# Kernel optimization log

Measured on AMD Instinct MI355X. Metric: run time of the kernel, lower is better.

## Reference

```python
import jax, jax.numpy as jnp
import numpy as np

N_EMBD = 512
HEAD_SIZE = 64
T = 4096
B = 4


def setup_inputs() -> dict:
    key = jax.random.key(0)
    kx, kq, kk, kv = jax.random.split(key, 4)
    x = jax.random.normal(kx, (B, T, N_EMBD), dtype=jnp.float32)
    # torch nn.Linear(n_embd, head_size, bias=False): weight [head_size, n_embd];
    # stored here transposed as [n_embd, head_size] so projection is x @ W.
    s = 1.0 / np.sqrt(N_EMBD)
    Wq = jax.random.uniform(kq, (N_EMBD, HEAD_SIZE), jnp.float32, -s, s)
    Wk = jax.random.uniform(kk, (N_EMBD, HEAD_SIZE), jnp.float32, -s, s)
    Wv = jax.random.uniform(kv, (N_EMBD, HEAD_SIZE), jnp.float32, -s, s)
    return {"x": x, "Wq": Wq, "Wk": Wk, "Wv": Wv}


def reference(x, Wq, Wk, Wv):
    Bq, Tq, C = x.shape
    q = x @ Wq  # [B,T,H]
    k = x @ Wk  # [B,T,H]
    v = x @ Wv  # [B,T,H]
    # NOTE: original scales by C**-0.5 with C = n_embd (input dim), not head_size.
    wei = jnp.einsum('bqh,bkh->bqk', q, k) * (C ** -0.5)  # [B,T,T]
    causal = jnp.tril(jnp.ones((Tq, Tq), dtype=bool))
    wei = jnp.where(causal, wei, -jnp.inf)
    wei = jax.nn.softmax(wei, axis=-1)
    # dropout p=0.0 -> identity (eval-mode deterministic baseline)
    out = jnp.einsum('bqk,bkh->bqh', wei, v)  # [B,T,H]
    return out
```

## Files before the change

kernel.cpp:

```cpp
#include <hip/hip_runtime.h>
#include <hip/hip_bf16.h>
#include <math.h>

#define T_SEQ 4096
#define NBATCH 4
#define C_EMB 512
#define HEAD 64
#define CHUNK 8
#define EPB 144

typedef __attribute__((ext_vector_type(8))) short short8;
typedef __attribute__((ext_vector_type(4))) short short4v;
typedef __attribute__((ext_vector_type(4))) float f32x4;

#define C2 (0.044194173824159216f * 1.44269504088896340736f)

__device__ __forceinline__ unsigned short f2bf(float f) {
    union { float f; unsigned u; } v; v.f = f;
    unsigned u = v.u;
    u += 0x7FFF + ((u >> 16) & 1);
    return (unsigned short)(u >> 16);
}
__device__ __forceinline__ unsigned pk2bf(float a, float b) {
    __hip_bfloat162 h = __float22bfloat162_rn(make_float2(a, b));
    return *(unsigned*)&h;
}
__device__ __forceinline__ float bf2f(unsigned short u) {
    union { unsigned u; float f; } v; v.u = ((unsigned)u) << 16;
    return v.f;
}

#define GLD_LDS16(gp, lp)                                                     \
    __builtin_amdgcn_global_load_lds(                                         \
        (const __attribute__((address_space(1))) void*)(gp),                  \
        (__attribute__((address_space(3))) void*)(lp), 16, 0, 0)

__global__ __launch_bounds__(64) void wcvt_kernel(
    const float* __restrict__ Wq, const float* __restrict__ Wk,
    const float* __restrict__ Wv, unsigned short* __restrict__ wt2)
{
    const int gid  = blockIdx.x * 64 + threadIdx.x;
    const int lane = gid & 63;
    int rest = gid >> 6;
    const int kc   = rest & 1; rest >>= 1;
    const int tile = rest % 12;
    const int c    = rest / 12;
    const float* W = (tile < 4) ? Wq : (tile < 8) ? Wk : Wv;
    const int n  = (tile & 3) * 16 + (lane & 15);
    const int k0 = c * 64 + kc * 32 + (lane >> 4) * 8;
    unsigned short tmp[8];
#pragma unroll
    for (int i = 0; i < 8; ++i) tmp[i] = f2bf(W[(size_t)(k0 + i) * HEAD + n]);
    *(short8*)(wt2 + (size_t)gid * 8) = *(short8*)tmp;
}

__global__ __launch_bounds__(512, 4) void proj_kernel(
    const float* __restrict__ x,
    const unsigned short* __restrict__ wt2,
    unsigned short* __restrict__ qout,
    unsigned short* __restrict__ kout,
    unsigned short* __restrict__ vt)
{
    __shared__ unsigned short Wl[2][12288];
    __shared__ unsigned short Xl[2][32][72];

    const int tid  = threadIdx.x;
    const int wave = tid >> 6;
    const int lane = tid & 63;
    const int l16  = lane & 15;
    const int quad = lane >> 4;
    const int row0 = blockIdx.x * 32;
    const int mq   = wave & 1;
    const int ng   = wave >> 1;

    const bool xst = tid < 256;
    const int xrow = tid >> 3;
    const int xc8  = (tid & 7) * 8;

    f32x4 acc[3];
#pragma unroll
    for (int j = 0; j < 3; ++j) acc[j] = (f32x4){0.f, 0.f, 0.f, 0.f};

#pragma unroll
    for (int m = 0; m < 3; ++m)
        GLD_LDS16(wt2 + (size_t)(m * 4096 + wave * 512 + lane * 8),
                  &Wl[0][m * 4096 + wave * 512]);
    if (xst) {
        const float* xs = x + (size_t)(row0 + xrow) * C_EMB + xc8;
        float4 a = *(const float4*)(xs);
        float4 b = *(const float4*)(xs + 4);
        int4 ai = make_int4((int)pk2bf(a.x, a.y), (int)pk2bf(a.z, a.w),
                            (int)pk2bf(b.x, b.y), (int)pk2bf(b.z, b.w));
        *(short8*)&Xl[0][xrow][xc8] = *(short8*)&ai;
    }
    __syncthreads();

    for (int c = 0; c < 8; ++c) {
        const int bb = c & 1;
        if (c < 7) {
            const int nb = bb ^ 1;
            const size_t g0 = (size_t)(c + 1) * 12288;
#pragma unroll
            for (int m = 0; m < 3; ++m)
                GLD_LDS16(wt2 + g0 + (size_t)(m * 4096 + wave * 512 + lane * 8),
                          &Wl[nb][m * 4096 + wave * 512]);
            if (xst) {
                const float* xs = x + (size_t)(row0 + xrow) * C_EMB + (c + 1) * 64 + xc8;
                float4 a = *(const float4*)(xs);
                float4 b = *(const float4*)(xs + 4);
                int4 ai = make_int4((int)pk2bf(a.x, a.y), (int)pk2bf(a.z, a.w),
                                    (int)pk2bf(b.x, b.y), (int)pk2bf(b.z, b.w));
                *(short8*)&Xl[nb][xrow][xc8] = *(short8*)&ai;
            }
        }

#pragma unroll
        for (int kc = 0; kc < 2; ++kc) {
            short8 a0 = *(const short8*)&Xl[bb][mq * 16 + l16][kc * 32 + quad * 8];
#pragma unroll
            for (int j = 0; j < 3; ++j) {
                const int ct = ng * 3 + j;
                short8 bfr = *(const short8*)&Wl[bb][(ct * 128 + kc * 64 + lane) * 8];
                acc[j] = __builtin_amdgcn_mfma_f32_16x16x32_bf16(a0, bfr, acc[j], 0, 0, 0);
            }
        }
        __syncthreads();
    }

    unsigned short (*Vsh)[40] = (unsigned short (*)[40]) & Xl[0][0][0];
#pragma unroll
    for (int j = 0; j < 3; ++j) {
        const int ct = ng * 3 + j;
        const int m  = ct >> 2;
        const int n  = ct & 3;
#pragma unroll
        for (int r = 0; r < 4; ++r) {
            const int row = row0 + mq * 16 + quad * 4 + r;
            if (m == 0)
                qout[(size_t)row * HEAD + n * 16 + l16] = f2bf(acc[j][r] * C2);
            else if (m == 1)
                kout[(size_t)row * HEAD + n * 16 + l16] = f2bf(acc[j][r]);
            else
                Vsh[n * 16 + l16][mq * 16 + quad * 4 + r] = f2bf(acc[j][r]);
        }
    }
    __syncthreads();
    if (tid < 256) {
        int h  = tid >> 2;
        int tc = (tid & 3) * 8;
        int b  = row0 >> 12;
        int t0 = row0 & (T_SEQ - 1);
        unsigned short* dst = vt + ((size_t)(b * HEAD + h)) * T_SEQ + t0 + tc;
        *(short8*)dst = *(const short8*)&Vsh[h][tc];
    }
}

__device__ __forceinline__ void stage_v8(unsigned short (*Vbuf)[72], int sr, int pos0,
                                         short8 v0) {
    *(short4v*)&Vbuf[sr][pos0]     = __builtin_shufflevector(v0, v0, 0, 1, 2, 3);
    *(short4v*)&Vbuf[sr][pos0 + 8] = __builtin_shufflevector(v0, v0, 4, 5, 6, 7);
}

__global__ __launch_bounds__(512, 4) void attn1_kernel(
    const unsigned short* __restrict__ qb,
    const unsigned short* __restrict__ kb,
    const unsigned short* __restrict__ vt,
    unsigned short* __restrict__ po,
    float* __restrict__ pl)
{
    __shared__ unsigned short Ks[2][64][72];
    __shared__ unsigned short Vs[2][64][72];

    const int tid  = threadIdx.x;
    const int wave = tid >> 6;
    const int lane = tid & 63;
    const int l16  = lane & 15;
    const int quad = lane >> 4;

    const int b = blockIdx.x / EPB;
    const int e = (EPB - 1) - (blockIdx.x % EPB);
    int g = 0;
#pragma unroll
    for (int gg = 1; gg < 8; ++gg) if (e >= 2 * gg * (gg + 1)) g = gg;
    const int rem = e - 2 * g * (g + 1);
    const int t   = rem / (g + 1);
    const int c   = rem - t * (g + 1);
    const int Q   = 4 * g + t;

    const size_t base = (size_t)b * T_SEQ;
    const int qrow0 = Q * 128 + wave * 16;
    const int qrow  = qrow0 + l16;
    short8 aq0 = *(const short8*)(qb + (base + qrow) * HEAD + quad * 8);
    short8 aq1 = *(const short8*)(qb + (base + qrow) * HEAD + 32 + quad * 8);

    float lacc = 0.f;
    f32x4 o[4];
#pragma unroll
    for (int n = 0; n < 4; ++n) o[n] = (f32x4){0.f, 0.f, 0.f, 0.f};

    const int nk  = 2 * Q + 2;
    const int kt0 = c * CHUNK;
    const int np  = min(CHUNK, nk - kt0);

    const int sr   = tid >> 3;
    const int scK  = (tid & 7) * 8;
    const int vc   = scK;
    const int pos0 = (vc & 32) + ((vc & 8) << 1) + ((vc & 16) >> 2);

    short8 kra, vra;
    {
        const int kbase = kt0 * 64;
        kra = *(const short8*)(kb + (base + kbase + sr) * HEAD + scK);
        vra = *(const short8*)(vt + ((size_t)(b * HEAD + sr)) * T_SEQ + kbase + vc);
    }
    *(short8*)&Ks[0][sr][scK] = kra;
    stage_v8(Vs[0], sr, pos0, vra);

    for (int p = 0; p < np; ++p) {
        const int cur = p & 1;
        const int kbase = (kt0 + p) * 64;
        __syncthreads();

        if (p + 1 < np) {
            const int nb = kbase + 64;
            kra = *(const short8*)(kb + (base + nb + sr) * HEAD + scK);
            vra = *(const short8*)(vt + ((size_t)(b * HEAD + sr)) * T_SEQ + nb + vc);
        }

        const bool live = (kbase <= qrow0 + 15);
        if (live) {
            f32x4 s[4];
            __builtin_amdgcn_s_setprio(1);
#pragma unroll
            for (int n = 0; n < 4; ++n) {
                short8 bk0 = *(const short8*)&Ks[cur][n * 16 + l16][quad * 8];
                short8 bk1 = *(const short8*)&Ks[cur][n * 16 + l16][32 + quad * 8];
                f32x4 accS = (f32x4){0.f, 0.f, 0.f, 0.f};
                accS = __builtin_amdgcn_mfma_f32_16x16x32_bf16(bk0, aq0, accS, 0, 0, 0);
                accS = __builtin_amdgcn_mfma_f32_16x16x32_bf16(bk1, aq1, accS, 0, 0, 0);
                s[n] = accS;
            }
            __builtin_amdgcn_s_setprio(0);

#pragma unroll
            for (int n = 0; n < 4; ++n)
#pragma unroll
                for (int r = 0; r < 4; ++r)
                    s[n][r] = __builtin_amdgcn_exp2f(s[n][r]);

            if (kbase + 63 > qrow0) {
                const int cb = kbase + quad * 4;
#pragma unroll
                for (int n = 0; n < 4; ++n)
#pragma unroll
                    for (int r = 0; r < 4; ++r)
                        if (cb + n * 16 + r > qrow) s[n][r] = 0.f;
            }

#pragma unroll
            for (int n = 0; n < 4; ++n)
                lacc += (s[n][0] + s[n][1]) + (s[n][2] + s[n][3]);

#pragma unroll
            for (int st = 0; st < 2; ++st) {
                int4 ai = make_int4(
                    (int)pk2bf(s[2 * st][0],     s[2 * st][1]),
                    (int)pk2bf(s[2 * st][2],     s[2 * st][3]),
                    (int)pk2bf(s[2 * st + 1][0], s[2 * st + 1][1]),
                    (int)pk2bf(s[2 * st + 1][2], s[2 * st + 1][3]));
                short8 af = *(short8*)&ai;
                __builtin_amdgcn_s_setprio(1);
#pragma unroll
                for (int n = 0; n < 4; ++n) {
                    short8 bv = *(const short8*)&Vs[cur][n * 16 + l16][32 * st + quad * 8];
                    o[n] = __builtin_amdgcn_mfma_f32_16x16x32_bf16(af, bv, o[n], 0, 0, 0);
                }
                __builtin_amdgcn_s_setprio(0);
            }
        }

        if (p + 1 < np) {
            const int nxt = cur ^ 1;
            *(short8*)&Ks[nxt][sr][scK] = kra;
            stage_v8(Vs[nxt], sr, pos0, vra);
        }
    }

    lacc += __shfl_xor(lacc, 16);
    lacc += __shfl_xor(lacc, 32);

    const int pid = blockIdx.x;
#pragma unroll
    for (int n = 0; n < 4; ++n)
#pragma unroll
        for (int r = 0; r < 4; ++r) {
            int lr = wave * 16 + quad * 4 + r;
            po[(size_t)pid * 8192 + lr * 64 + n * 16 + l16] = f2bf(o[n][r]);
        }
    if (quad == 0)
        pl[pid * 128 + wave * 16 + l16] = lacc;
}

__global__ __launch_bounds__(256) void combine_kernel(
    const unsigned short* __restrict__ po, const float* __restrict__ pl,
    float* __restrict__ out)
{
    const int gth = blockIdx.x * 256 + threadIdx.x;
    const int h8  = gth & 7;
    const int row = gth >> 3;
    const int lr  = row & 127;
    const int Q   = (row >> 7) & 31;
    const int b   = row >> 12;
    const int g   = Q >> 2;
    const int rem = Q & 3;
    const int nc  = g + 1;
    const int e0  = 2 * g * (g + 1) + rem * (g + 1);
    const int pid0 = b * EPB + (EPB - 1 - e0);

    float l = 0.f;
    float acc[8];
#pragma unroll
    for (int i = 0; i < 8; ++i) acc[i] = 0.f;
    for (int cc = 0; cc < nc; ++cc) {
        l += pl[(pid0 - cc) * 128 + lr];
        short8 p8 = *(const short8*)(po + (size_t)(pid0 - cc) * 8192 + lr * 64 + h8 * 8);
#pragma unroll
        for (int i = 0; i < 8; ++i) acc[i] += bf2f((unsigned short)p8[i]);
    }
    float inv = 1.f / l;
    float4 r0 = make_float4(acc[0] * inv, acc[1] * inv, acc[2] * inv, acc[3] * inv);
    float4 r1 = make_float4(acc[4] * inv, acc[5] * inv, acc[6] * inv, acc[7] * inv);
    float* dst = out + (size_t)gth * 8;
    *(float4*)dst       = r0;
    *(float4*)(dst + 4) = r1;
}

extern "C" void kernel_launch(void* const* d_in, const int* in_sizes, int n_in,
                              void* d_out, int out_size, void* d_ws, size_t ws_size,
                              hipStream_t stream) {
    const float* x  = (const float*)d_in[0];
    const float* Wq = (const float*)d_in[1];
    const float* Wk = (const float*)d_in[2];
    const float* Wv = (const float*)d_in[3];
    float* out = (float*)d_out;

    char* ws = (char*)d_ws;
    unsigned short* qb = (unsigned short*)(ws);
    unsigned short* kb = (unsigned short*)(ws + (2u << 20));
    unsigned short* vt = (unsigned short*)(ws + (4u << 20));
    unsigned short* wt2 = (unsigned short*)(ws + (6u << 20));
    float* pl = (float*)(ws + (6u << 20) + 196608);
    unsigned short* po = (unsigned short*)(ws + (6u << 20) + 196608 + 294912);

    wcvt_kernel<<<dim3(192), dim3(64), 0, stream>>>(Wq, Wk, Wv, wt2);
    proj_kernel<<<dim3(512), dim3(512), 0, stream>>>(x, wt2, qb, kb, vt);
    attn1_kernel<<<dim3(NBATCH * EPB), dim3(512), 0, stream>>>(qb, kb, vt, po, pl);
    combine_kernel<<<dim3(512), dim3(256), 0, stream>>>(po, pl, out);
}
```

Measured before the change: 110.8 us.

## Have each attention wave process two 16-row query groups with 256-thread blocks

```diff
diff --git a/kernel.cpp b/kernel.cpp
--- a/kernel.cpp
+++ b/kernel.cpp
@@ -155,13 +155,15 @@
     }
 }
 
-__device__ __forceinline__ void stage_v8(unsigned short (*Vbuf)[72], int sr, int pos0,
-                                         short8 v0) {
-    *(short4v*)&Vbuf[sr][pos0]     = __builtin_shufflevector(v0, v0, 0, 1, 2, 3);
-    *(short4v*)&Vbuf[sr][pos0 + 8] = __builtin_shufflevector(v0, v0, 4, 5, 6, 7);
-}
-
-__global__ __launch_bounds__(512, 4) void attn1_kernel(
+__device__ __forceinline__ void stage_v(unsigned short (*Vbuf)[72], int sr, int phiA,
+                                        short8 v0, short8 v1) {
+    *(short4v*)&Vbuf[sr][phiA]      = __builtin_shufflevector(v0, v0, 0, 1, 2, 3);
+    *(short4v*)&Vbuf[sr][phiA + 8]  = __builtin_shufflevector(v0, v0, 4, 5, 6, 7);
+    *(short4v*)&Vbuf[sr][phiA + 16] = __builtin_shufflevector(v1, v1, 0, 1, 2, 3);
+    *(short4v*)&Vbuf[sr][phiA + 24] = __builtin_shufflevector(v1, v1, 4, 5, 6, 7);
+}
+
+__global__ __launch_bounds__(256) void attn1_kernel(
     const unsigned short* __restrict__ qb,
     const unsigned short* __restrict__ kb,
     const unsigned short* __restrict__ vt,
@@ -188,33 +190,40 @@
     const int Q   = 4 * g + t;
 
     const size_t base = (size_t)b * T_SEQ;
-    const int qrow0 = Q * 128 + wave * 16;
-    const int qrow  = qrow0 + l16;
-    short8 aq0 = *(const short8*)(qb + (base + qrow) * HEAD + quad * 8);
-    short8 aq1 = *(const short8*)(qb + (base + qrow) * HEAD + 32 + quad * 8);
-
-    float lacc = 0.f;
-    f32x4 o[4];
-#pragma unroll
-    for (int n = 0; n < 4; ++n) o[n] = (f32x4){0.f, 0.f, 0.f, 0.f};
+    const int qrow0 = Q * 128 + wave * 32;
+    short8 aq[2][2];
+#pragma unroll
+    for (int qg = 0; qg < 2; ++qg) {
+        const int qr = qrow0 + qg * 16 + l16;
+        aq[qg][0] = *(const short8*)(qb + (base + qr) * HEAD + quad * 8);
+        aq[qg][1] = *(const short8*)(qb + (base + qr) * HEAD + 32 + quad * 8);
+    }
+
+    float lacc[2] = {0.f, 0.f};
+    f32x4 o[2][4];
+#pragma unroll
+    for (int qg = 0; qg < 2; ++qg)
+#pragma unroll
+        for (int n = 0; n < 4; ++n) o[qg][n] = (f32x4){0.f, 0.f, 0.f, 0.f};
 
     const int nk  = 2 * Q + 2;
     const int kt0 = c * CHUNK;
     const int np  = min(CHUNK, nk - kt0);
 
-    const int sr   = tid >> 3;
-    const int scK  = (tid & 7) * 8;
-    const int vc   = scK;
-    const int pos0 = (vc & 32) + ((vc & 8) << 1) + ((vc & 16) >> 2);
-
-    short8 kra, vra;
+    const int sr   = tid >> 2;
+    const int sc   = (tid & 3) * 16;
+    const int phiA = (sc & 32) + ((sc & 16) >> 2);
+
+    short8 kra, krb, vra, vrb;
     {
         const int kbase = kt0 * 64;
-        kra = *(const short8*)(kb + (base + kbase + sr) * HEAD + scK);
-        vra = *(const short8*)(vt + ((size_t)(b * HEAD + sr)) * T_SEQ + kbase + vc);
-    }
-    *(short8*)&Ks[0][sr][scK] = kra;
-    stage_v8(Vs[0], sr, pos0, vra);
+        const unsigned short* ksrc = kb + (base + kbase + sr) * HEAD + sc;
+        const unsigned short* vsrc = vt + ((size_t)(b * HEAD + sr)) * T_SEQ + kbase + sc;
+        kra = *(const short8*)(ksrc);     krb = *(const short8*)(ksrc + 8);
+        vra = *(const short8*)(vsrc);     vrb = *(const short8*)(vsrc + 8);
+    }
+    *(short8*)&Ks[0][sr][sc]     = kra;  *(short8*)&Ks[0][sr][sc + 8] = krb;
+    stage_v(Vs[0], sr, phiA, vra, vrb);
 
     for (int p = 0; p < np; ++p) {
         const int cur = p & 1;
@@ -223,82 +232,108 @@
 
         if (p + 1 < np) {
             const int nb = kbase + 64;
-            kra = *(const short8*)(kb + (base + nb + sr) * HEAD + scK);
-            vra = *(const short8*)(vt + ((size_t)(b * HEAD + sr)) * T_SEQ + nb + vc);
-        }
-
-        const bool live = (kbase <= qrow0 + 15);
+            const unsigned short* ksrc = kb + (base + nb + sr) * HEAD + sc;
+            const unsigned short* vsrc = vt + ((size_t)(b * HEAD + sr)) * T_SEQ + nb + sc;
+            kra = *(const short8*)(ksrc);  krb = *(const short8*)(ksrc + 8);
+            vra = *(const short8*)(vsrc);  vrb = *(const short8*)(vsrc + 8);
+        }
+
+        const bool live = (kbase <= qrow0 + 31);
         if (live) {
-            f32x4 s[4];
+            f32x4 s[2][4];
             __builtin_amdgcn_s_setprio(1);
 #pragma unroll
             for (int n = 0; n < 4; ++n) {
                 short8 bk0 = *(const short8*)&Ks[cur][n * 16 + l16][quad * 8];
                 short8 bk1 = *(const short8*)&Ks[cur][n * 16 + l16][32 + quad * 8];
-                f32x4 accS = (f32x4){0.f, 0.f, 0.f, 0.f};
-                accS = __builtin_amdgcn_mfma_f32_16x16x32_bf16(bk0, aq0, accS, 0, 0, 0);
-                accS = __builtin_amdgcn_mfma_f32_16x16x32_bf16(bk1, aq1, accS, 0, 0, 0);
-                s[n] = accS;
+#pragma unroll
+                for (int qg = 0; qg < 2; ++qg) {
+                    f32x4 accS = (f32x4){0.f, 0.f, 0.f, 0.f};
+                    accS = __builtin_amdgcn_mfma_f32_16x16x32_bf16(bk0, aq[qg][0], accS, 0, 0, 0);
+                    accS = __builtin_amdgcn_mfma_f32_16x16x32_bf16(bk1, aq[qg][1], accS, 0, 0, 0);
+                    s[qg][n] = accS;
+                }
             }
             __builtin_amdgcn_s_setprio(0);
 
 #pragma unroll
-            for (int n = 0; n < 4; ++n)
-#pragma unroll
-                for (int r = 0; r < 4; ++r)
-                    s[n][r] = __builtin_amdgcn_exp2f(s[n][r]);
+            for (int qg = 0; qg < 2; ++qg)
+#pragma unroll
+                for (int n = 0; n < 4; ++n)
+#pragma unroll
+                    for (int r = 0; r < 4; ++r)
+                        s[qg][n][r] = __builtin_amdgcn_exp2f(s[qg][n][r]);
 
             if (kbase + 63 > qrow0) {
                 const int cb = kbase + quad * 4;
 #pragma unroll
+                for (int qg = 0; qg < 2; ++qg) {
+                    const int qr = qrow0 + qg * 16 + l16;
+#pragma unroll
+                    for (int n = 0; n < 4; ++n)
+#pragma unroll
+                        for (int r = 0; r < 4; ++r)
+                            if (cb + n * 16 + r > qr) s[qg][n][r] = 0.f;
+                }
+            }
+
+#pragma unroll
+            for (int qg = 0; qg < 2; ++qg)
+#pragma unroll
                 for (int n = 0; n < 4; ++n)
-#pragma unroll
-                    for (int r = 0; r < 4; ++r)
-                        if (cb + n * 16 + r > qrow) s[n][r] = 0.f;
-            }
-
-#pragma unroll
-            for (int n = 0; n < 4; ++n)
-                lacc += (s[n][0] + s[n][1]) + (s[n][2] + s[n][3]);
-
-#pragma unroll
-            for (int st = 0; st < 2; ++st) {
-                int4 ai = make_int4(
-                    (int)pk2bf(s[2 * st][0],     s[2 * st][1]),
-                    (int)pk2bf(s[2 * st][2],     s[2 * st][3]),
-                    (int)pk2bf(s[2 * st + 1][0], s[2 * st + 1][1]),
-                    (int)pk2bf(s[2 * st + 1][2], s[2 * st + 1][3]));
-                short8 af = *(short8*)&ai;
-                __builtin_amdgcn_s_setprio(1);
+                    lacc[qg] += (s[qg][n][0] + s[qg][n][1]) + (s[qg][n][2] + s[qg][n][3]);
+
+            short8 pa[2][2];
+#pragma unroll
+            for (int qg = 0; qg < 2; ++qg)
+#pragma unroll
+                for (int st = 0; st < 2; ++st) {
+                    int4 ai = make_int4(
+                        (int)pk2bf(s[qg][2 * st][0],     s[qg][2 * st][1]),
+                        (int)pk2bf(s[qg][2 * st][2],     s[qg][2 * st][3]),
+                        (int)pk2bf(s[qg][2 * st + 1][0], s[qg][2 * st + 1][1]),
+                        (int)pk2bf(s[qg][2 * st + 1][2], s[qg][2 * st + 1][3]));
+                    pa[qg][st] = *(short8*)&ai;
+                }
+
+            __builtin_amdgcn_s_setprio(1);
+#pragma unroll
+            for (int st = 0; st < 2; ++st)
 #pragma unroll
                 for (int n = 0; n < 4; ++n) {
                     short8 bv = *(const short8*)&Vs[cur][n * 16 + l16][32 * st + quad * 8];
-                    o[n] = __builtin_amdgcn_mfma_f32_16x16x32_bf16(af, bv, o[n], 0, 0, 0);
+                    o[0][n] = __builtin_amdgcn_mfma_f32_16x16x32_bf16(pa[0][st], bv, o[0][n], 0, 0, 0);
+                    o[1][n] = __builtin_amdgcn_mfma_f32_16x16x32_bf16(pa[1][st], bv, o[1][n], 0, 0, 0);
                 }
-                __builtin_amdgcn_s_setprio(0);
-            }
+            __builtin_amdgcn_s_setprio(0);
         }
 
         if (p + 1 < np) {
             const int nxt = cur ^ 1;
-            *(short8*)&Ks[nxt][sr][scK] = kra;
-            stage_v8(Vs[nxt], sr, pos0, vra);
-        }
-    }
-
-    lacc += __shfl_xor(lacc, 16);
-    lacc += __shfl_xor(lacc, 32);
+            *(short8*)&Ks[nxt][sr][sc]     = kra;  *(short8*)&Ks[nxt][sr][sc + 8] = krb;
+            stage_v(Vs[nxt], sr, phiA, vra, vrb);
+        }
+    }
+
+#pragma unroll
+    for (int qg = 0; qg < 2; ++qg) {
+        lacc[qg] += __shfl_xor(lacc[qg], 16);
+        lacc[qg] += __shfl_xor(lacc[qg], 32);
+    }
 
     const int pid = blockIdx.x;
 #pragma unroll
-    for (int n = 0; n < 4; ++n)
-#pragma unroll
-        for (int r = 0; r < 4; ++r) {
-            int lr = wave * 16 + quad * 4 + r;
-            po[(size_t)pid * 8192 + lr * 64 + n * 16 + l16] = f2bf(o[n][r]);
-        }
-    if (quad == 0)
-        pl[pid * 128 + wave * 16 + l16] = lacc;
+    for (int qg = 0; qg < 2; ++qg) {
+#pragma unroll
+        for (int n = 0; n < 4; ++n)
+#pragma unroll
+            for (int r = 0; r < 4; ++r) {
+                int lr = wave * 32 + qg * 16 + quad * 4 + r;
+                po[(size_t)pid * 8192 + lr * 64 + n * 16 + l16] = f2bf(o[qg][n][r]);
+            }
+        if (quad == 0)
+            pl[pid * 128 + wave * 32 + qg * 16 + l16] = lacc[qg];
+    }
 }
 
 __global__ __launch_bounds__(256) void combine_kernel(
@@ -354,6 +389,6 @@
 
     wcvt_kernel<<<dim3(192), dim3(64), 0, stream>>>(Wq, Wk, Wv, wt2);
     proj_kernel<<<dim3(512), dim3(512), 0, stream>>>(x, wt2, qb, kb, vt);
-    attn1_kernel<<<dim3(NBATCH * EPB), dim3(512), 0, stream>>>(qb, kb, vt, po, pl);
+    attn1_kernel<<<dim3(NBATCH * EPB), dim3(256), 0, stream>>>(qb, kb, vt, po, pl);
     combine_kernel<<<dim3(512), dim3(256), 0, stream>>>(po, pl, out);
 }
```

Result: slower. 116.2 us (+4.9%).

## Fuse split-K combine into attention kernel via last-block atomic counter

Applied to the files above, without the earlier changes.

```diff
diff --git a/kernel.cpp b/kernel.cpp
--- a/kernel.cpp
+++ b/kernel.cpp
@@ -37,9 +37,11 @@
 
 __global__ __launch_bounds__(64) void wcvt_kernel(
     const float* __restrict__ Wq, const float* __restrict__ Wk,
-    const float* __restrict__ Wv, unsigned short* __restrict__ wt2)
+    const float* __restrict__ Wv, unsigned short* __restrict__ wt2,
+    int* __restrict__ cnt)
 {
     const int gid  = blockIdx.x * 64 + threadIdx.x;
+    if (gid < NBATCH * 32) cnt[gid] = 0;
     const int lane = gid & 63;
     int rest = gid >> 6;
     const int kc   = rest & 1; rest >>= 1;
@@ -166,10 +168,13 @@
     const unsigned short* __restrict__ kb,
     const unsigned short* __restrict__ vt,
     unsigned short* __restrict__ po,
-    float* __restrict__ pl)
+    float* __restrict__ pl,
+    int* __restrict__ cnt,
+    float* __restrict__ out)
 {
     __shared__ unsigned short Ks[2][64][72];
     __shared__ unsigned short Vs[2][64][72];
+    __shared__ int lastf;
 
     const int tid  = threadIdx.x;
     const int wave = tid >> 6;
@@ -186,6 +191,8 @@
     const int t   = rem / (g + 1);
     const int c   = rem - t * (g + 1);
     const int Q   = 4 * g + t;
+    const int nc  = g + 1;
+    const int e0  = 2 * g * (g + 1) + t * (g + 1);
 
     const size_t base = (size_t)b * T_SEQ;
     const int qrow0 = Q * 128 + wave * 16;
@@ -289,7 +296,23 @@
     lacc += __shfl_xor(lacc, 16);
     lacc += __shfl_xor(lacc, 32);
 
-    const int pid = blockIdx.x;
+    if (nc == 1) {
+        float invr[4];
+#pragma unroll
+        for (int r = 0; r < 4; ++r)
+            invr[r] = 1.f / __shfl(lacc, quad * 4 + r);
+#pragma unroll
+        for (int n = 0; n < 4; ++n)
+#pragma unroll
+            for (int r = 0; r < 4; ++r) {
+                const int row = qrow0 + quad * 4 + r;
+                out[((size_t)(b * T_SEQ + row)) * HEAD + n * 16 + l16] =
+                    o[n][r] * invr[r];
+            }
+        return;
+    }
+
+    const int pid = b * EPB + e0 + c;
 #pragma unroll
     for (int n = 0; n < 4; ++n)
 #pragma unroll
@@ -299,40 +322,36 @@
         }
     if (quad == 0)
         pl[pid * 128 + wave * 16 + l16] = lacc;
-}
-
-__global__ __launch_bounds__(256) void combine_kernel(
-    const unsigned short* __restrict__ po, const float* __restrict__ pl,
-    float* __restrict__ out)
-{
-    const int gth = blockIdx.x * 256 + threadIdx.x;
-    const int h8  = gth & 7;
-    const int row = gth >> 3;
-    const int lr  = row & 127;
-    const int Q   = (row >> 7) & 31;
-    const int b   = row >> 12;
-    const int g   = Q >> 2;
-    const int rem = Q & 3;
-    const int nc  = g + 1;
-    const int e0  = 2 * g * (g + 1) + rem * (g + 1);
-    const int pid0 = b * EPB + (EPB - 1 - e0);
-
-    float l = 0.f;
-    float acc[8];
-#pragma unroll
-    for (int i = 0; i < 8; ++i) acc[i] = 0.f;
-    for (int cc = 0; cc < nc; ++cc) {
-        l += pl[(pid0 - cc) * 128 + lr];
-        short8 p8 = *(const short8*)(po + (size_t)(pid0 - cc) * 8192 + lr * 64 + h8 * 8);
-#pragma unroll
-        for (int i = 0; i < 8; ++i) acc[i] += bf2f((unsigned short)p8[i]);
-    }
-    float inv = 1.f / l;
-    float4 r0 = make_float4(acc[0] * inv, acc[1] * inv, acc[2] * inv, acc[3] * inv);
-    float4 r1 = make_float4(acc[4] * inv, acc[5] * inv, acc[6] * inv, acc[7] * inv);
-    float* dst = out + (size_t)gth * 8;
-    *(float4*)dst       = r0;
-    *(float4*)(dst + 4) = r1;
+
+    __threadfence();
+    __syncthreads();
+    if (tid == 0)
+        lastf = (atomicAdd(&cnt[b * 32 + Q], 1) == nc - 1);
+    __syncthreads();
+    if (!lastf) return;
+    __threadfence();
+
+#pragma unroll
+    for (int oo = 0; oo < 2; ++oo) {
+        const int oct = tid * 2 + oo;
+        const int h8  = oct & 7;
+        const int lr  = oct >> 3;
+        float l = 0.f;
+        float a8[8];
+#pragma unroll
+        for (int i = 0; i < 8; ++i) a8[i] = 0.f;
+        for (int cc = 0; cc < nc; ++cc) {
+            const int pp = b * EPB + e0 + cc;
+            l += pl[pp * 128 + lr];
+            short8 p8 = *(const short8*)(po + (size_t)pp * 8192 + lr * 64 + h8 * 8);
+#pragma unroll
+            for (int i = 0; i < 8; ++i) a8[i] += bf2f((unsigned short)p8[i]);
+        }
+        float inv = 1.f / l;
+        float* dst = out + ((size_t)(b * T_SEQ + Q * 128 + lr)) * HEAD + h8 * 8;
+        *(float4*)dst       = make_float4(a8[0] * inv, a8[1] * inv, a8[2] * inv, a8[3] * inv);
+        *(float4*)(dst + 4) = make_float4(a8[4] * inv, a8[5] * inv, a8[6] * inv, a8[7] * inv);
+    }
 }
 
 extern "C" void kernel_launch(void* const* d_in, const int* in_sizes, int n_in,
@@ -350,10 +369,10 @@
     unsigned short* vt = (unsigned short*)(ws + (4u << 20));
     unsigned short* wt2 = (unsigned short*)(ws + (6u << 20));
     float* pl = (float*)(ws + (6u << 20) + 196608);
-    unsigned short* po = (unsigned short*)(ws + (6u << 20) + 196608 + 294912);
-
-    wcvt_kernel<<<dim3(192), dim3(64), 0, stream>>>(Wq, Wk, Wv, wt2);
+    int* cnt = (int*)(ws + (6u << 20) + 196608 + 294912);
+    unsigned short* po = (unsigned short*)(ws + (6u << 20) + 196608 + 294912 + 512);
+
+    wcvt_kernel<<<dim3(192), dim3(64), 0, stream>>>(Wq, Wk, Wv, wt2, cnt);
     proj_kernel<<<dim3(512), dim3(512), 0, stream>>>(x, wt2, qb, kb, vt);
-    attn1_kernel<<<dim3(NBATCH * EPB), dim3(512), 0, stream>>>(qb, kb, vt, po, pl);
-    combine_kernel<<<dim3(512), dim3(256), 0, stream>>>(po, pl, out);
-}
+    attn1_kernel<<<dim3(NBATCH * EPB), dim3(512), 0, stream>>>(qb, kb, vt, po, pl, cnt, out);
+}
```

New measurement: 310.2 us. 180% more time.
